# Kernel optimization log

Measured on AMD Instinct MI355X. Metric: run time of the kernel, lower is better.

The kernel has to match this reference:

```python
import jax, jax.numpy as jnp
import numpy as np
from jax import lax

VTH = 0.5
GRAD_WIN = 0.5
CDECAY = 0.5
VDECAY = 0.75

@jax.custom_vjp
def pseudo_spike(v):
    # PseudoSpikeRect: heaviside fwd, rectangular surrogate grad bwd
    return (v > VTH).astype(v.dtype)

def _ps_fwd(v):
    return pseudo_spike(v), v

def _ps_bwd(v, g):
    return (g * (jnp.abs(v - VTH) < GRAD_WIN).astype(g.dtype),)

pseudo_spike.defvjp(_ps_fwd, _ps_bwd)

def conv2d(x, w, b):
    y = lax.conv_general_dilated(x, w, (1, 1), 'VALID',
                                 dimension_numbers=('NCHW', 'OIHW', 'NCHW'))
    return y + b[None, :, None, None]

def lif(psp, state):
    # CUBA-LIF: current decay + integrate, voltage decay with spike reset, threshold
    cur, volt, spk = state
    cur = CDECAY * cur + psp
    volt = VDECAY * volt * (1.0 - spk) + cur
    spk = pseudo_spike(volt)
    return spk, (cur, volt, spk)

def setup_inputs() -> dict:
    key = jax.random.key(0)
    ks = jax.random.split(key, 16)
    B, T = 64, 200
    c1, c2, c3 = 64, 128, 256
    s = lambda k, shape, scale: jax.random.normal(k, shape, jnp.float32) * scale
    return {
        'input_data': jax.random.normal(ks[0], (B, 1, 10, 10, T), jnp.float32),
        'conv1_w': s(ks[1], (c1, 1, 3, 3), 0.3), 'conv1_b': s(ks[2], (c1,), 0.1),
        'conv2_w': s(ks[3], (c2, c1, 3, 3), 0.05), 'conv2_b': s(ks[4], (c2,), 0.1),
        'conv3_w': s(ks[5], (c3, c2, 3, 3), 0.03), 'conv3_b': s(ks[6], (c3,), 0.1),
        'tc_w': s(ks[7], (3, c3, c3), 0.06), 'tc_b': s(ks[8], (3, c3), 0.1),
        'rec_w': s(ks[9], (c3, c3), 0.06), 'rec_b': s(ks[10], (c3,), 0.1),
        'fc1_w': s(ks[11], (128, c3), 0.06), 'fc1_b': s(ks[12], (128,), 0.1),
        'fc2_w': s(ks[13], (2, 128), 0.09),
        'ts_weights': jnp.ones((T, 1), jnp.float32) / T,
    }

def reference(input_data, conv1_w, conv1_b, conv2_w, conv2_b, conv3_w, conv3_b,
              tc_w, tc_b, rec_w, rec_b, fc1_w, fc1_b, fc2_w, ts_weights):
    B = input_data.shape[0]
    c1, c2, c3 = conv1_w.shape[0], conv2_w.shape[0], conv3_w.shape[0]
    f1 = fc1_w.shape[0]

    def zs(shape):
        z = jnp.zeros(shape, input_data.dtype)
        return (z, z, z)

    carry0 = (zs((B, c1, 8, 8)), zs((B, c2, 6, 6)), zs((B, c3, 1, 1)),
              zs((B, c3)), zs((B, c3)), zs((B, f1)),
              jnp.zeros((3, B, c3), input_data.dtype),  # temporal buffer, idx0 = newest
              jnp.int32(0))
    xs = jnp.moveaxis(input_data, -1, 0)  # [T, B, 1, 10, 10]

    def step_fn(carry, xw):
        c1_st, c2_st, c3_st, tc_st, r_st, f_st, buf, step = carry
        x, w = xw
        s1, c1_st = lif(conv2d(x, conv1_w, conv1_b), c1_st)       # [B,c1,8,8]
        s2, c2_st = lif(conv2d(s1, conv2_w, conv2_b), c2_st)      # [B,c2,6,6]
        p = s2.reshape(B, c2, 3, 2, 3, 2).mean(axis=(3, 5))       # AvgPool2d(2) -> [B,c2,3,3]
        s3, c3_st = lif(conv2d(p, conv3_w, conv3_b), c3_st)       # [B,c3,1,1]
        flat = s3.reshape(B, -1)                                   # [B,c3]
        buf = jnp.concatenate([flat[None], buf[:2]], axis=0)
        # temporal conv: tap i applies to spike at time t-i, only if it exists
        psp = jnp.zeros_like(flat)
        for i in range(3):
            tap = buf[i] @ tc_w[i].T + tc_b[i]
            psp = psp + jnp.where(step >= i, 1.0, 0.0).astype(tap.dtype) * tap
        s_tc, tc_st = lif(psp, tc_st)
        # recurrent cell: identity feedforward + linear on previous spike
        psp_r = s_tc + r_st[2] @ rec_w.T + rec_b
        s_r, r_st = lif(psp_r, r_st)
        s_f, f_st = lif(s_r @ fc1_w.T + fc1_b, f_st)
        out = (s_f @ fc2_w.T) * w  # w = ts_weights[step], shape [1]
        return (c1_st, c2_st, c3_st, tc_st, r_st, f_st, buf, step + 1), out

    _, outs = lax.scan(step_fn, carry0, (xs, ts_weights))
    return outs.sum(axis=0)  # [B, 2]
```

## Files before the change

kernel.cpp:

```cpp
#include <hip/hip_runtime.h>


#define B_   64
#define T_   200
#define TCB_ 50

__device__ __forceinline__ void lif32(float psp, float& cur, float& volt, float& spk) {
#pragma clang fp contract(off)
    cur  = __fadd_rn(__fmul_rn(0.5f, cur), psp);
    volt = __fadd_rn(__fmul_rn(__fmul_rn(0.75f, volt), __fsub_rn(1.0f, spk)), cur);
    spk  = (volt > 0.5f) ? 1.0f : 0.0f;
}

__global__ void k_setup(const float* __restrict__ w2, const float* __restrict__ w3,
                        const float* __restrict__ tcw, const float* __restrict__ recw,
                        const float* __restrict__ fw,
                        float* __restrict__ w2T, float* __restrict__ w3T,
                        float* __restrict__ tcT, float* __restrict__ recT,
                        float* __restrict__ fc1T) {
    int idx = blockIdx.x * 256 + threadIdx.x;
    if (idx < 73728) { int o = idx & 127, k = idx >> 7; w2T[idx] = w2[o * 576 + k]; return; }
    idx -= 73728;
    if (idx < 294912) { int o = idx & 255, k = idx >> 8; w3T[idx] = w3[o * 1152 + k]; return; }
    idx -= 294912;
    if (idx < 196608) { int tap = idx >> 16, r = idx & 65535; int o = r & 255, k = r >> 8;
                        tcT[idx] = tcw[tap * 65536 + o * 256 + k]; return; }
    idx -= 196608;
    if (idx < 65536) { int o = idx & 255, k = idx >> 8; recT[idx] = recw[o * 256 + k]; return; }
    idx -= 65536;
    if (idx < 32768) { int o = idx & 127, k = idx >> 7; fc1T[idx] = fw[o * 256 + k]; return; }
}

__global__ __launch_bounds__(256) void k_conv1(const float* __restrict__ x,
                                               const float* __restrict__ w1,
                                               const float* __restrict__ b1,
                                               unsigned char* __restrict__ s1c,
                                               float* __restrict__ st1,
                                               int t0, int TC, int first) {
    int idx = blockIdx.x * 256 + threadIdx.x;
    int xx = idx & 7, yy = (idx >> 3) & 7, o = (idx >> 6) & 63, b = idx >> 12;
    float w[9];
#pragma unroll
    for (int i = 0; i < 9; i++) w[i] = w1[o * 9 + i];
    float bias = b1[o];
    const float* xb = x + (size_t)b * 20000;
    unsigned char* sb = s1c + (size_t)b * TC * 4096 + (o << 6) + (yy << 3) + xx;
    float cur, volt, spk;
    if (first) { cur = 0.f; volt = 0.f; spk = 0.f; }
    else { cur = st1[idx]; volt = st1[262144 + idx]; spk = st1[524288 + idx]; }
    for (int tl = 0; tl < TC; tl += 4) {
        int t = t0 + tl;
        float a0 = 0.f, a1 = 0.f, a2 = 0.f, a3 = 0.f;
#pragma unroll
        for (int i = 0; i < 3; i++) {
#pragma unroll
            for (int j = 0; j < 3; j++) {
                float4 v = *(const float4*)&xb[((yy + i) * 10 + xx + j) * T_ + t];
                float wv = w[i * 3 + j];
                a0 = fmaf(wv, v.x, a0); a1 = fmaf(wv, v.y, a1);
                a2 = fmaf(wv, v.z, a2); a3 = fmaf(wv, v.w, a3);
            }
        }
        float accs[4] = {a0, a1, a2, a3};
#pragma unroll
        for (int q = 0; q < 4; q++) {
            float psp = __fadd_rn(accs[q], bias);
            lif32(psp, cur, volt, spk);
            sb[(size_t)(tl + q) * 4096] = (unsigned char)spk;
        }
    }
    st1[idx] = cur; st1[262144 + idx] = volt; st1[524288 + idx] = spk;
}

__global__ __launch_bounds__(384) void k_conv2(const unsigned char* __restrict__ s1c,
                                               const float* __restrict__ w2T,
                                               const float* __restrict__ b2,
                                               float* __restrict__ psp2c) {
    __shared__ float a_s[4096];
    int blk = blockIdx.x;
    int tid = threadIdx.x;
    const unsigned int* src4 = (const unsigned int*)(s1c + (size_t)blk * 4096);
    for (int i = tid; i < 1024; i += 384) {
        unsigned int u = src4[i];
        a_s[4 * i + 0] = (float)(u & 0xff);
        a_s[4 * i + 1] = (float)((u >> 8) & 0xff);
        a_s[4 * i + 2] = (float)((u >> 16) & 0xff);
        a_s[4 * i + 3] = (float)(u >> 24);
    }
    __syncthreads();
    int oc = tid & 127;
    int yg = tid >> 7;
    int y0 = 2 * yg;
    float acc0[6], acc1[6];
#pragma unroll
    for (int xq = 0; xq < 6; xq++) { acc0[xq] = 0.f; acc1[xq] = 0.f; }
    const float* wb = w2T + oc;
    for (int c = 0; c < 64; c++) {
        const float* sc = &a_s[c * 64 + y0 * 8];
        float row[4][8];
#pragma unroll
        for (int ry = 0; ry < 4; ry++) {
            float4 fa = *(const float4*)(sc + ry * 8);
            float4 fb = *(const float4*)(sc + ry * 8 + 4);
            row[ry][0] = fa.x; row[ry][1] = fa.y; row[ry][2] = fa.z; row[ry][3] = fa.w;
            row[ry][4] = fb.x; row[ry][5] = fb.y; row[ry][6] = fb.z; row[ry][7] = fb.w;
        }
        float w[9];
#pragma unroll
        for (int q = 0; q < 9; q++) w[q] = wb[(size_t)(c * 9 + q) * 128];
#pragma unroll
        for (int i = 0; i < 3; i++)
#pragma unroll
            for (int j = 0; j < 3; j++) {
                float wv = w[i * 3 + j];
#pragma unroll
                for (int xq = 0; xq < 6; xq++) {
                    acc0[xq] = fmaf(wv, row[i][xq + j], acc0[xq]);
                    acc1[xq] = fmaf(wv, row[i + 1][xq + j], acc1[xq]);
                }
            }
    }
    float bv = b2[oc];
    float* dst0 = psp2c + (size_t)blk * 4608 + (size_t)oc * 36 + y0 * 6;
    float* dst1 = dst0 + 6;
#pragma unroll
    for (int xq = 0; xq < 6; xq++) {
        dst0[xq] = __fadd_rn(acc0[xq], bv);
        dst1[xq] = __fadd_rn(acc1[xq], bv);
    }
}

__global__ __launch_bounds__(256) void k_lif2pool(const float* __restrict__ psp2c,
                                                  float* __restrict__ pc,
                                                  float* __restrict__ st2,
                                                  int TC, int first) {
    int idx = blockIdx.x * 256 + threadIdx.x;
    int px = idx % 3; int r = idx / 3; int py = r % 3; r /= 3;
    int o = r & 127, b = r >> 7;
    const float* pb = psp2c + (size_t)b * TC * 4608 + o * 36;
    float* pd = pc + (size_t)b * TC * 1152 + o * 9 + py * 3 + px;
    int off0 = (2 * py) * 6 + 2 * px, off1 = off0 + 6;
    float c0, c1, c2, c3, v0, v1, v2, v3, s0, s1, s2, s3;
    if (first) {
        c0 = c1 = c2 = c3 = v0 = v1 = v2 = v3 = s0 = s1 = s2 = s3 = 0.f;
    } else {
        c0 = st2[idx];              c1 = st2[73728 + idx];
        c2 = st2[147456 + idx];     c3 = st2[221184 + idx];
        v0 = st2[294912 + idx];     v1 = st2[368640 + idx];
        v2 = st2[442368 + idx];     v3 = st2[516096 + idx];
        s0 = st2[589824 + idx];     s1 = st2[663552 + idx];
        s2 = st2[737280 + idx];     s3 = st2[811008 + idx];
    }
    for (int tl = 0; tl < TC; tl++) {
        const float* pt = pb + (size_t)tl * 4608;
        float2 ra = *(const float2*)(pt + off0);
        float2 rb = *(const float2*)(pt + off1);
        lif32(ra.x, c0, v0, s0);
        lif32(ra.y, c1, v1, s1);
        lif32(rb.x, c2, v2, s2);
        lif32(rb.y, c3, v3, s3);
        pd[(size_t)tl * 1152] = __fmul_rn(0.25f, __fadd_rn(__fadd_rn(__fadd_rn(s0, s1), s2), s3));
    }
    st2[idx] = c0;           st2[73728 + idx] = c1;
    st2[147456 + idx] = c2;  st2[221184 + idx] = c3;
    st2[294912 + idx] = v0;  st2[368640 + idx] = v1;
    st2[442368 + idx] = v2;  st2[516096 + idx] = v3;
    st2[589824 + idx] = s0;  st2[663552 + idx] = s1;
    st2[737280 + idx] = s2;  st2[811008 + idx] = s3;
}

__global__ __launch_bounds__(256) void k_conv3(const float* __restrict__ pc,
                                               const float* __restrict__ w3T,
                                               const float* __restrict__ b3,
                                               float* __restrict__ psp3c) {
    __shared__ float a_s[4 * 1152];
    int row0 = blockIdx.x * 4;
    int tid = threadIdx.x;
    int oq = tid & 63, mg = tid >> 6;
    for (int idx = tid; idx < 4 * 1152; idx += 256) {
        int m = idx / 1152, k = idx - m * 1152;
        a_s[idx] = pc[(size_t)(row0 + m) * 1152 + k];
    }
    __syncthreads();
    float acc[4] = {0.f, 0.f, 0.f, 0.f};
    const float* as_row = &a_s[mg * 1152];
#pragma unroll 4
    for (int k = 0; k < 1152; k++) {
        float4 wv = *(const float4*)&w3T[(size_t)k * 256 + (oq << 2)];
        float am = as_row[k];
        acc[0] = fmaf(wv.x, am, acc[0]);
        acc[1] = fmaf(wv.y, am, acc[1]);
        acc[2] = fmaf(wv.z, am, acc[2]);
        acc[3] = fmaf(wv.w, am, acc[3]);
    }
    float* dst = psp3c + (size_t)(row0 + mg) * 256 + (oq << 2);
#pragma unroll
    for (int oo = 0; oo < 4; oo++)
        dst[oo] = __fadd_rn(acc[oo], b3[(oq << 2) + oo]);
}

__global__ __launch_bounds__(256) void k_scan3(const float* __restrict__ psp3c,
                                               unsigned char* __restrict__ s3u8,
                                               float* __restrict__ st3,
                                               int t0, int TC, int first) {
    int idx = blockIdx.x * 256 + threadIdx.x;
    int b = idx >> 8, n = idx & 255;
    float cur, volt, spk;
    if (first) { cur = 0.f; volt = 0.f; spk = 0.f; }
    else { cur = st3[idx]; volt = st3[16384 + idx]; spk = st3[32768 + idx]; }
    for (int tl = 0; tl < TC; tl++) {
        lif32(psp3c[(size_t)(b * TC + tl) * 256 + n], cur, volt, spk);
        s3u8[((size_t)b * T_ + t0 + tl) * 256 + n] = (unsigned char)spk;
    }
    st3[idx] = cur; st3[16384 + idx] = volt; st3[32768 + idx] = spk;
}

__global__ __launch_bounds__(256) void k_tc(const unsigned char* __restrict__ s3u8,
                                            const float* __restrict__ tcT,
                                            const float* __restrict__ tc_b,
                                            float* __restrict__ ptcc, int t0) {
    __shared__ float a_s[16 * 256];
    int crow0 = blockIdx.x * 16;
    int tid = threadIdx.x;
    int oq = tid & 63, mg = tid >> 6;
    float psum[4][4];
#pragma unroll
    for (int oo = 0; oo < 4; oo++)
#pragma unroll
        for (int mi = 0; mi < 4; mi++) psum[oo][mi] = 0.f;
    for (int tap = 0; tap < 3; tap++) {
        __syncthreads();
        for (int idx = tid; idx < 16 * 256; idx += 256) {
            int m = idx >> 8, k = idx & 255;
            int crow = crow0 + m;
            int b = crow / TCB_, tl = crow - b * TCB_;
            int t = t0 + tl;
            float v = 0.f;
            if (t >= tap) v = (float)s3u8[((size_t)b * T_ + t - tap) * 256 + k];
            a_s[idx] = v;
        }
        __syncthreads();
        float acc[4][4];
#pragma unroll
        for (int oo = 0; oo < 4; oo++)
#pragma unroll
            for (int mi = 0; mi < 4; mi++) acc[oo][mi] = 0.f;
        const float* wbase = tcT + (size_t)tap * 65536 + (oq << 2);
        for (int k = 0; k < 256; k++) {
            float4 wv = *(const float4*)(wbase + (size_t)k * 256);
            float w4[4] = {wv.x, wv.y, wv.z, wv.w};
            float am[4];
#pragma unroll
            for (int mi = 0; mi < 4; mi++) am[mi] = a_s[(mg * 4 + mi) * 256 + k];
#pragma unroll
            for (int oo = 0; oo < 4; oo++)
#pragma unroll
                for (int mi = 0; mi < 4; mi++)
                    acc[oo][mi] = fmaf(w4[oo], am[mi], acc[oo][mi]);
        }
#pragma unroll
        for (int mi = 0; mi < 4; mi++) {
            int crow = crow0 + mg * 4 + mi;
            int b = crow / TCB_, tl = crow - b * TCB_;
            int t = t0 + tl;
            float g = (t >= tap) ? 1.0f : 0.0f;
#pragma unroll
            for (int oo = 0; oo < 4; oo++) {
                int oc = (oq << 2) + oo;
                float tap_f = __fadd_rn(acc[oo][mi], tc_b[tap * 256 + oc]);
                psum[oo][mi] = __fadd_rn(psum[oo][mi], __fmul_rn(g, tap_f));
            }
        }
    }
#pragma unroll
    for (int mi = 0; mi < 4; mi++) {
        int crow = crow0 + mg * 4 + mi;
        float* dst = ptcc + (size_t)crow * 256 + (oq << 2);
#pragma unroll
        for (int oo = 0; oo < 4; oo++) dst[oo] = psum[oo][mi];
    }
}

__global__ __launch_bounds__(256) void k_scan_tc(const float* __restrict__ ptcc,
                                                 unsigned char* __restrict__ s_tc8,
                                                 float* __restrict__ st_tc,
                                                 int t0, int first) {
    int idx = blockIdx.x * 256 + threadIdx.x;
    int b = idx >> 8, n = idx & 255;
    float cur, volt, spk;
    if (first) { cur = 0.f; volt = 0.f; spk = 0.f; }
    else { cur = st_tc[idx]; volt = st_tc[16384 + idx]; spk = st_tc[32768 + idx]; }
    for (int tl = 0; tl < TCB_; tl++) {
        lif32(ptcc[(size_t)(b * TCB_ + tl) * 256 + n], cur, volt, spk);
        s_tc8[((size_t)b * T_ + t0 + tl) * 256 + n] = (unsigned char)spk;
    }
    st_tc[idx] = cur; st_tc[16384 + idx] = volt; st_tc[32768 + idx] = spk;
}

__global__ __launch_bounds__(512, 1) void k_rec(const unsigned char* __restrict__ s_tc8,
                                                const float* __restrict__ rec_w,
                                                const float* __restrict__ rec_b,
                                                unsigned char* __restrict__ s_r8) {
    __shared__ __align__(16) float spk_s[2][256];
    __shared__ float acc_s[256];
    int b = blockIdx.x;
    int tid = threadIdx.x;
    int o = tid & 255, half = tid >> 8;
    float w[128];
#pragma unroll
    for (int j = 0; j < 32; j++) {
        float4 v = *(const float4*)&rec_w[(size_t)o * 256 + (half << 7) + 4 * j];
        w[4 * j + 0] = v.x; w[4 * j + 1] = v.y;
        w[4 * j + 2] = v.z; w[4 * j + 3] = v.w;
    }
#pragma unroll
    for (int k = 0; k < 128; k++) asm volatile("" : "+v"(w[k]));
    if (half == 0) spk_s[0][o] = 0.f;
    float cur = 0.f, volt = 0.f, spk = 0.f;
    float rb = rec_b[o];
    const unsigned char* stp = s_tc8 + (size_t)b * T_ * 256 + o;
    unsigned char* srp = s_r8 + (size_t)b * T_ * 256 + o;
    __syncthreads();
    int p = 0;
    for (int t = 0; t < T_; t++) {
        if (half == 0) {
            const float* sp = spk_s[p];
            float acc = 0.f;
#pragma unroll
            for (int k = 0; k < 128; k += 4) {
                float4 sv = *(const float4*)&sp[k];
                acc = fmaf(sv.x, w[k + 0], acc);
                acc = fmaf(sv.y, w[k + 1], acc);
                acc = fmaf(sv.z, w[k + 2], acc);
                acc = fmaf(sv.w, w[k + 3], acc);
            }
            acc_s[o] = acc;
        }
        __syncthreads();
        if (half == 1) {
            float stc = (float)stp[(size_t)t * 256];
            const float* sp = spk_s[p] + 128;
            float acc = acc_s[o];
#pragma unroll
            for (int k = 0; k < 128; k += 4) {
                float4 sv = *(const float4*)&sp[k];
                acc = fmaf(sv.x, w[k + 0], acc);
                acc = fmaf(sv.y, w[k + 1], acc);
                acc = fmaf(sv.z, w[k + 2], acc);
                acc = fmaf(sv.w, w[k + 3], acc);
            }
            float psp = __fadd_rn(__fadd_rn(stc, acc), rb);
            lif32(psp, cur, volt, spk);
            srp[(size_t)t * 256] = (unsigned char)spk;
            spk_s[p ^ 1][o] = spk;
        }
        __syncthreads();
        p ^= 1;
    }
}

__global__ __launch_bounds__(256) void k_fc1(const unsigned char* __restrict__ s_r8,
                                             const float* __restrict__ fc1T,
                                             const float* __restrict__ fc1_b,
                                             float* __restrict__ pfc, int t0) {
    __shared__ float a_s[16 * 256];
    int crow0 = blockIdx.x * 16;
    int tid = threadIdx.x;
    int oq = tid & 31, mg = tid >> 5;
    float acc[4][2];
#pragma unroll
    for (int oo = 0; oo < 4; oo++) { acc[oo][0] = 0.f; acc[oo][1] = 0.f; }
    for (int idx = tid; idx < 16 * 256; idx += 256) {
        int m = idx >> 8, k = idx & 255;
        int crow = crow0 + m;
        int b = crow / TCB_, tl = crow - b * TCB_;
        a_s[idx] = (float)s_r8[((size_t)b * T_ + t0 + tl) * 256 + k];
    }
    __syncthreads();
    for (int k = 0; k < 256; k++) {
        float4 wv = *(const float4*)&fc1T[(size_t)k * 128 + (oq << 2)];
        float w4[4] = {wv.x, wv.y, wv.z, wv.w};
        float a0 = a_s[(mg * 2 + 0) * 256 + k];
        float a1 = a_s[(mg * 2 + 1) * 256 + k];
#pragma unroll
        for (int oo = 0; oo < 4; oo++) {
            acc[oo][0] = fmaf(w4[oo], a0, acc[oo][0]);
            acc[oo][1] = fmaf(w4[oo], a1, acc[oo][1]);
        }
    }
#pragma unroll
    for (int mi = 0; mi < 2; mi++) {
        float* dst = pfc + (size_t)(crow0 + mg * 2 + mi) * 128 + (oq << 2);
#pragma unroll
        for (int oo = 0; oo < 4; oo++)
            dst[oo] = __fadd_rn(acc[oo][mi], fc1_b[(oq << 2) + oo]);
    }
}

__global__ __launch_bounds__(256) void k_scan_f(const float* __restrict__ pfc,
                                                unsigned char* __restrict__ s_f8,
                                                float* __restrict__ st_f,
                                                int t0, int first) {
    int idx = blockIdx.x * 256 + threadIdx.x;
    int b = idx >> 7, n = idx & 127;
    float cur, volt, spk;
    if (first) { cur = 0.f; volt = 0.f; spk = 0.f; }
    else { cur = st_f[idx]; volt = st_f[8192 + idx]; spk = st_f[16384 + idx]; }
    for (int tl = 0; tl < TCB_; tl++) {
        lif32(pfc[(size_t)(b * TCB_ + tl) * 128 + n], cur, volt, spk);
        s_f8[((size_t)b * T_ + t0 + tl) * 128 + n] = (unsigned char)spk;
    }
    st_f[idx] = cur; st_f[8192 + idx] = volt; st_f[16384 + idx] = spk;
}

__global__ __launch_bounds__(128) void k_final(const unsigned char* __restrict__ s_f8,
                                               const float* __restrict__ ts,
                                               const float* __restrict__ fc2,
                                               float* __restrict__ out) {
    __shared__ double q_s[128];
    int b = blockIdx.x, k = threadIdx.x;
    double q = 0.0;
    const unsigned char* sf = s_f8 + (size_t)b * T_ * 128 + k;
    for (int t = 0; t < T_; t++) q = fma((double)ts[t], (double)sf[(size_t)t * 128], q);
    q_s[k] = q;
    __syncthreads();
    if (k < 2) {
        double o = 0.0;
        for (int kk = 0; kk < 128; kk++) o = fma((double)fc2[k * 128 + kk], q_s[kk], o);
        out[b * 2 + k] = (float)o;
    }
}

extern "C" void kernel_launch(void* const* d_in, const int* in_sizes, int n_in,
                              void* d_out, int out_size, void* d_ws, size_t ws_size,
                              hipStream_t stream) {
    const float* x       = (const float*)d_in[0];
    const float* conv1_w = (const float*)d_in[1];
    const float* conv1_b = (const float*)d_in[2];
    const float* conv2_w = (const float*)d_in[3];
    const float* conv2_b = (const float*)d_in[4];
    const float* conv3_w = (const float*)d_in[5];
    const float* conv3_b = (const float*)d_in[6];
    const float* tc_w    = (const float*)d_in[7];
    const float* tc_b    = (const float*)d_in[8];
    const float* rec_w   = (const float*)d_in[9];
    const float* rec_b   = (const float*)d_in[10];
    const float* fc1_w   = (const float*)d_in[11];
    const float* fc1_b   = (const float*)d_in[12];
    const float* fc2_w   = (const float*)d_in[13];
    const float* ts_w    = (const float*)d_in[14];
    float* out = (float*)d_out;
    (void)in_sizes; (void)n_in; (void)out_size;

    char* base = (char*)d_ws;
    float* w2T  = (float*)(base + 0);
    float* w3T  = (float*)(base + 294912);
    float* tcT  = (float*)(base + 1474560);
    float* recT = (float*)(base + 2260992);
    float* fc1T = (float*)(base + 2523136);
    float* st1  = (float*)(base + 2654208);
    float* st2  = (float*)(base + 5799936);
    float* st3  = (float*)(base + 9338880);
    float* st_tc= (float*)(base + 9535488);
    float* st_f = (float*)(base + 9732096);
    unsigned char* s3u8  = (unsigned char*)(base + 9830400);
    unsigned char* s_tc8 = (unsigned char*)(base + 13107200);
    unsigned char* s_r8  = (unsigned char*)(base + 16384000);
    unsigned char* s_f8  = (unsigned char*)(base + 19660800);

    const size_t PERS = 21299200;
    const size_t PER_T = 1802240;
    int TCF;
    if      (ws_size >= PERS + 40 * PER_T) TCF = 40;
    else if (ws_size >= PERS + 20 * PER_T) TCF = 20;
    else if (ws_size >= PERS +  8 * PER_T) TCF = 8;
    else                                   TCF = 4;
    int NCH = T_ / TCF;
    char* cb = base + PERS;
    float* psp2c = (float*)(cb);
    float* psp3c = (float*)(cb + (size_t)TCF * 1179648);
    float* pc    = (float*)(cb + (size_t)TCF * (1179648 + 65536));
    unsigned char* s1c = (unsigned char*)(cb + (size_t)TCF * (1179648 + 65536 + 294912));
    float* ptcc = (float*)(cb);
    float* pfc  = (float*)(cb + 3276800);

    k_setup<<<2592, 256, 0, stream>>>(conv2_w, conv3_w, tc_w, rec_w, fc1_w,
                                      w2T, w3T, tcT, recT, fc1T);
    for (int ch = 0; ch < NCH; ch++) {
        int t0 = ch * TCF;
        int first = (ch == 0) ? 1 : 0;
        k_conv1<<<1024, 256, 0, stream>>>(x, conv1_w, conv1_b, s1c, st1, t0, TCF, first);
        k_conv2<<<B_ * TCF, 384, 0, stream>>>(s1c, w2T, conv2_b, psp2c);
        k_lif2pool<<<288, 256, 0, stream>>>(psp2c, pc, st2, TCF, first);
        k_conv3<<<B_ * TCF / 4, 256, 0, stream>>>(pc, w3T, conv3_b, psp3c);
        k_scan3<<<64, 256, 0, stream>>>(psp3c, s3u8, st3, t0, TCF, first);
    }
    for (int bc = 0; bc < T_ / TCB_; bc++) {
        int t0 = bc * TCB_;
        k_tc<<<B_ * TCB_ / 16, 256, 0, stream>>>(s3u8, tcT, tc_b, ptcc, t0);
        k_scan_tc<<<64, 256, 0, stream>>>(ptcc, s_tc8, st_tc, t0, (bc == 0) ? 1 : 0);
    }
    k_rec<<<64, 512, 0, stream>>>(s_tc8, rec_w, rec_b, s_r8);
    for (int bc = 0; bc < T_ / TCB_; bc++) {
        int t0 = bc * TCB_;
        k_fc1<<<B_ * TCB_ / 16, 256, 0, stream>>>(s_r8, fc1T, fc1_b, pfc, t0);
        k_scan_f<<<32, 256, 0, stream>>>(pfc, s_f8, st_f, t0, (bc == 0) ? 1 : 0);
    }
    k_final<<<64, 128, 0, stream>>>(s_f8, ts_w, fc2_w, out);
}
```

Before: 2.434 ms.

## Process two timesteps per conv2 block and switch psp2 to channel-minor layout

```diff
diff --git a/kernel.cpp b/kernel.cpp
--- a/kernel.cpp
+++ b/kernel.cpp
@@ -75,58 +75,73 @@
 __global__ __launch_bounds__(384) void k_conv2(const unsigned char* __restrict__ s1c,
                                                const float* __restrict__ w2T,
                                                const float* __restrict__ b2,
-                                               float* __restrict__ psp2c) {
-    __shared__ float a_s[4096];
+                                               float* __restrict__ psp2c, int TC) {
+    __shared__ float s_s[2][4096];
     int blk = blockIdx.x;
+    int th = TC >> 1;
+    int b = blk / th, tp = blk - b * th;
+    int tl0 = 2 * tp;
     int tid = threadIdx.x;
-    const unsigned int* src4 = (const unsigned int*)(s1c + (size_t)blk * 4096);
-    for (int i = tid; i < 1024; i += 384) {
-        unsigned int u = src4[i];
-        a_s[4 * i + 0] = (float)(u & 0xff);
-        a_s[4 * i + 1] = (float)((u >> 8) & 0xff);
-        a_s[4 * i + 2] = (float)((u >> 16) & 0xff);
-        a_s[4 * i + 3] = (float)(u >> 24);
+#pragma unroll
+    for (int h = 0; h < 2; h++) {
+        const unsigned int* src4 = (const unsigned int*)(s1c + (size_t)(b * TC + tl0 + h) * 4096);
+        for (int i = tid; i < 1024; i += 384) {
+            unsigned int u = src4[i];
+            s_s[h][4 * i + 0] = (float)(u & 0xff);
+            s_s[h][4 * i + 1] = (float)((u >> 8) & 0xff);
+            s_s[h][4 * i + 2] = (float)((u >> 16) & 0xff);
+            s_s[h][4 * i + 3] = (float)(u >> 24);
+        }
     }
     __syncthreads();
     int oc = tid & 127;
     int yg = tid >> 7;
     int y0 = 2 * yg;
-    float acc0[6], acc1[6];
-#pragma unroll
-    for (int xq = 0; xq < 6; xq++) { acc0[xq] = 0.f; acc1[xq] = 0.f; }
+    float a0[2][6], a1[2][6];
+#pragma unroll
+    for (int h = 0; h < 2; h++)
+#pragma unroll
+        for (int xq = 0; xq < 6; xq++) { a0[h][xq] = 0.f; a1[h][xq] = 0.f; }
     const float* wb = w2T + oc;
     for (int c = 0; c < 64; c++) {
-        const float* sc = &a_s[c * 64 + y0 * 8];
-        float row[4][8];
-#pragma unroll
-        for (int ry = 0; ry < 4; ry++) {
-            float4 fa = *(const float4*)(sc + ry * 8);
-            float4 fb = *(const float4*)(sc + ry * 8 + 4);
-            row[ry][0] = fa.x; row[ry][1] = fa.y; row[ry][2] = fa.z; row[ry][3] = fa.w;
-            row[ry][4] = fb.x; row[ry][5] = fb.y; row[ry][6] = fb.z; row[ry][7] = fb.w;
-        }
         float w[9];
 #pragma unroll
         for (int q = 0; q < 9; q++) w[q] = wb[(size_t)(c * 9 + q) * 128];
 #pragma unroll
-        for (int i = 0; i < 3; i++)
-#pragma unroll
-            for (int j = 0; j < 3; j++) {
-                float wv = w[i * 3 + j];
-#pragma unroll
-                for (int xq = 0; xq < 6; xq++) {
-                    acc0[xq] = fmaf(wv, row[i][xq + j], acc0[xq]);
-                    acc1[xq] = fmaf(wv, row[i + 1][xq + j], acc1[xq]);
+        for (int h = 0; h < 2; h++) {
+            const float* sc = &s_s[h][c * 64 + y0 * 8];
+            float row[4][8];
+#pragma unroll
+            for (int ry = 0; ry < 4; ry++) {
+                float4 fa = *(const float4*)(sc + ry * 8);
+                float4 fb = *(const float4*)(sc + ry * 8 + 4);
+                row[ry][0] = fa.x; row[ry][1] = fa.y; row[ry][2] = fa.z; row[ry][3] = fa.w;
+                row[ry][4] = fb.x; row[ry][5] = fb.y; row[ry][6] = fb.z; row[ry][7] = fb.w;
+            }
+#pragma unroll
+            for (int i = 0; i < 3; i++)
+#pragma unroll
+                for (int j = 0; j < 3; j++) {
+                    float wv = w[i * 3 + j];
+#pragma unroll
+                    for (int xq = 0; xq < 6; xq++) {
+                        a0[h][xq] = fmaf(wv, row[i][xq + j], a0[h][xq]);
+                        a1[h][xq] = fmaf(wv, row[i + 1][xq + j], a1[h][xq]);
+                    }
                 }
-            }
+        }
     }
     float bv = b2[oc];
-    float* dst0 = psp2c + (size_t)blk * 4608 + (size_t)oc * 36 + y0 * 6;
-    float* dst1 = dst0 + 6;
-#pragma unroll
-    for (int xq = 0; xq < 6; xq++) {
-        dst0[xq] = __fadd_rn(acc0[xq], bv);
-        dst1[xq] = __fadd_rn(acc1[xq], bv);
+#pragma unroll
+    for (int h = 0; h < 2; h++) {
+        float* base = psp2c + (size_t)(b * TC + tl0 + h) * 4608;
+        float* d0 = base + (size_t)(y0 * 6) * 128 + oc;
+        float* d1 = base + (size_t)((y0 + 1) * 6) * 128 + oc;
+#pragma unroll
+        for (int xq = 0; xq < 6; xq++) {
+            d0[(size_t)xq * 128] = __fadd_rn(a0[h][xq], bv);
+            d1[(size_t)xq * 128] = __fadd_rn(a1[h][xq], bv);
+        }
     }
 }
 
@@ -135,11 +150,17 @@
                                                   float* __restrict__ st2,
                                                   int TC, int first) {
     int idx = blockIdx.x * 256 + threadIdx.x;
-    int px = idx % 3; int r = idx / 3; int py = r % 3; r /= 3;
-    int o = r & 127, b = r >> 7;
-    const float* pb = psp2c + (size_t)b * TC * 4608 + o * 36;
-    float* pd = pc + (size_t)b * TC * 1152 + o * 9 + py * 3 + px;
-    int off0 = (2 * py) * 6 + 2 * px, off1 = off0 + 6;
+    int oc = idx & 127;
+    int r = idx >> 7;
+    int pos = r % 9;
+    int b = r / 9;
+    int py = pos / 3, px = pos - py * 3;
+    const float* pb = psp2c + (size_t)b * TC * 4608;
+    int off00 = ((2 * py) * 6 + 2 * px) * 128 + oc;
+    int off01 = ((2 * py) * 6 + 2 * px + 1) * 128 + oc;
+    int off10 = ((2 * py + 1) * 6 + 2 * px) * 128 + oc;
+    int off11 = ((2 * py + 1) * 6 + 2 * px + 1) * 128 + oc;
+    float* pd = pc + (size_t)b * TC * 1152 + oc * 9 + pos;
     float c0, c1, c2, c3, v0, v1, v2, v3, s0, s1, s2, s3;
     if (first) {
         c0 = c1 = c2 = c3 = v0 = v1 = v2 = v3 = s0 = s1 = s2 = s3 = 0.f;
@@ -153,12 +174,14 @@
     }
     for (int tl = 0; tl < TC; tl++) {
         const float* pt = pb + (size_t)tl * 4608;
-        float2 ra = *(const float2*)(pt + off0);
-        float2 rb = *(const float2*)(pt + off1);
-        lif32(ra.x, c0, v0, s0);
-        lif32(ra.y, c1, v1, s1);
-        lif32(rb.x, c2, v2, s2);
-        lif32(rb.y, c3, v3, s3);
+        float p0 = pt[off00];
+        float p1 = pt[off01];
+        float p2 = pt[off10];
+        float p3 = pt[off11];
+        lif32(p0, c0, v0, s0);
+        lif32(p1, c1, v1, s1);
+        lif32(p2, c2, v2, s2);
+        lif32(p3, c3, v3, s3);
         pd[(size_t)tl * 1152] = __fmul_rn(0.25f, __fadd_rn(__fadd_rn(__fadd_rn(s0, s1), s2), s3));
     }
     st2[idx] = c0;           st2[73728 + idx] = c1;
@@ -490,7 +513,7 @@
         int t0 = ch * TCF;
         int first = (ch == 0) ? 1 : 0;
         k_conv1<<<1024, 256, 0, stream>>>(x, conv1_w, conv1_b, s1c, st1, t0, TCF, first);
-        k_conv2<<<B_ * TCF, 384, 0, stream>>>(s1c, w2T, conv2_b, psp2c);
+        k_conv2<<<B_ * TCF / 2, 384, 0, stream>>>(s1c, w2T, conv2_b, psp2c, TCF);
         k_lif2pool<<<288, 256, 0, stream>>>(psp2c, pc, st2, TCF, first);
         k_conv3<<<B_ * TCF / 4, 256, 0, stream>>>(pc, w3T, conv3_b, psp3c);
         k_scan3<<<64, 256, 0, stream>>>(psp3c, s3u8, st3, t0, TCF, first);
```

After: 2.430 ms. No clear change (-0.2%).
